# Kernel optimization log

Measured on AMD Instinct MI355X. Metric: run time of the kernel, lower is better.

Reference implementation:

```python
import jax, jax.numpy as jnp
import numpy as np

B, C, N = 2, 512, 2048
HEADS, DIM_HEAD, SCALE = 16, 64, 8.0
H_DIM = HEADS * DIM_HEAD
EPS = 1e-12  # F.normalize default eps


def setup_inputs() -> dict:
    key = jax.random.key(0)
    ks = jax.random.split(key, 5)
    x = jax.random.normal(ks[0], (B, C, N), dtype=jnp.float32)
    Wqkv = jax.random.normal(ks[1], (3 * H_DIM, C), dtype=jnp.float32) * (1.0 / np.sqrt(C))
    q_scale = jnp.ones((DIM_HEAD,), dtype=jnp.float32)
    k_scale = jnp.ones((DIM_HEAD,), dtype=jnp.float32)
    Wout = jax.random.normal(ks[2], (C, H_DIM), dtype=jnp.float32) * (1.0 / np.sqrt(H_DIM))
    bout = jax.random.normal(ks[3], (C,), dtype=jnp.float32) * 0.01
    return {"x": x, "Wqkv": Wqkv, "q_scale": q_scale, "k_scale": k_scale,
            "Wout": Wout, "bout": bout}


def _l2norm(t):
    # F.normalize(t, dim=-1): t / max(||t||, eps)
    n = jnp.sqrt(jnp.sum(t * t, axis=-1, keepdims=True))
    return t / jnp.maximum(n, EPS)


def reference(x, Wqkv, q_scale, k_scale, Wout, bout):
    # 1x1 conv == pointwise matmul over channel dim
    qkv = jnp.einsum('oc,bcn->bon', Wqkv, x)              # [B, 3*H_DIM, N]
    q, k, v = jnp.split(qkv, 3, axis=1)
    # unflatten channels -> [B, H, D, N]
    def to_heads(t):
        return t.reshape(B, HEADS, DIM_HEAD, N)
    q, k, v = map(to_heads, (q, k, v))
    # cosine attention: l2-normalize q,k over head dim, apply learned per-dim scales
    q = _l2norm(q.transpose(0, 1, 3, 2)) * q_scale        # [B, H, N, D]
    k = _l2norm(k.transpose(0, 1, 3, 2)) * k_scale        # [B, H, N, D]
    sim = jnp.einsum('bhid,bhjd->bhij', q, k) * SCALE     # [B, H, N, N]
    attn = jax.nn.softmax(sim, axis=-1)
    out = jnp.einsum('bhij,bhdj->bhid', attn, v)          # [B, H, N, D]
    out = out.transpose(0, 1, 3, 2).reshape(B, H_DIM, N)  # b h n d -> b (h d) n
    return jnp.einsum('oc,bcn->bon', Wout, out) + bout[None, :, None]
```

## Files before the change

### kernel.cpp

```cpp
#include <hip/hip_runtime.h>
#include <hip/hip_bf16.h>

#define BATCH 2
#define CCH   512
#define NSEQ  2048
#define HEADS 16
#define DHEAD 64
#define HDIM  1024
#define ODIM  3072
#define SCALE 8.0f

typedef short short8 __attribute__((ext_vector_type(8)));
typedef float float4v __attribute__((ext_vector_type(4)));

__device__ __forceinline__ float bf2f(unsigned short b) {
    return __uint_as_float(((unsigned int)b) << 16);
}
__device__ __forceinline__ unsigned short f2bf(float f) {
    unsigned int u = __float_as_uint(f);
    return (unsigned short)((u + 0x7FFFu + ((u >> 16) & 1u)) >> 16);
}

typedef __attribute__((address_space(1))) const void* as1_cvp;
typedef __attribute__((address_space(3))) void* as3_vp;
__device__ __forceinline__ void cp16(const void* g, void* l) {
    __builtin_amdgcn_global_load_lds((as1_cvp)g, (as3_vp)l, 16, 0, 0);
}

__global__ __launch_bounds__(64) void k_prep(const float* __restrict__ qs,
                                             const float* __restrict__ ks,
                                             float* __restrict__ M) {
    int lane = threadIdx.x;
    float p = fabsf(qs[lane] * ks[lane]);
#pragma unroll
    for (int off = 1; off < 64; off <<= 1) p = fmaxf(p, __shfl_xor(p, off));
    if (lane == 0) *M = SCALE * p;
}

__global__ __launch_bounds__(256) void k_convert_w(
    const float* __restrict__ Wqkv, const float* __restrict__ Wout,
    unsigned short* __restrict__ Wqkvb, unsigned short* __restrict__ Woutb) {
    int i4 = (blockIdx.x * 256 + threadIdx.x) * 4;
    const float* src; unsigned short* dst; int idx;
    if (i4 < ODIM * CCH) { src = Wqkv; dst = Wqkvb; idx = i4; }
    else { src = Wout; dst = Woutb; idx = i4 - ODIM * CCH; }
    float4 v = *(const float4*)(src + idx);
    ushort4 o;
    o.x = f2bf(v.x); o.y = f2bf(v.y); o.z = f2bf(v.z); o.w = f2bf(v.w);
    *(ushort4*)(dst + idx) = o;
}

__global__ __launch_bounds__(256) void k_transpose_x(
    const float* __restrict__ x, unsigned short* __restrict__ xt) {
    __shared__ unsigned short t[64][65];
    const int b = blockIdx.z, c0 = blockIdx.y * 64, n0 = blockIdx.x * 64;
    const int tr = threadIdx.x >> 6, tc = threadIdx.x & 63;
    const float* xs = x + (size_t)b * CCH * NSEQ;
    unsigned short* xd = xt + (size_t)b * NSEQ * CCH;
#pragma unroll
    for (int r = 0; r < 16; ++r) {
        int c = r * 4 + tr;
        t[c][tc] = f2bf(xs[(size_t)(c0 + c) * NSEQ + n0 + tc]);
    }
    __syncthreads();
#pragma unroll
    for (int r = 0; r < 16; ++r) {
        int n = r * 4 + tr;
        xd[(size_t)(n0 + n) * CCH + c0 + tc] = t[tc][n];
    }
}

__global__ __launch_bounds__(256) void k_gemm_qkv(
    const unsigned short* __restrict__ W, const unsigned short* __restrict__ xt,
    const float* __restrict__ qs, const float* __restrict__ ks,
    unsigned short* __restrict__ qh, unsigned short* __restrict__ kh,
    unsigned short* __restrict__ vb) {
    constexpr int K = CCH, N = NSEQ;
    __shared__ __align__(16) short lsA[128 * 64];
    __shared__ __align__(16) short lsB[128 * 64];
    const int tid = threadIdx.x, wave = tid >> 6, lane = tid & 63;
    const int l15 = lane & 15, quad = lane >> 4;
    const int n0 = blockIdx.x * 128, m0 = blockIdx.y * 128, z = blockIdx.z;
    const short* Ab = (const short*)W + (size_t)m0 * K;
    const short* Bb = (const short*)xt + ((size_t)z * N + n0) * K;
    const int wm = wave >> 1, wn = wave & 1;
    const int cswz = (((tid & 7) ^ ((tid >> 3) & 7))) * 8;
    const int sw7 = (l15 & 7);

    float4v acc[4][4];
#pragma unroll
    for (int i = 0; i < 4; ++i)
#pragma unroll
        for (int j = 0; j < 4; ++j) acc[i][j] = (float4v){0.f, 0.f, 0.f, 0.f};

    for (int k0 = 0; k0 < K; k0 += 64) {
#pragma unroll
        for (int it = 0; it < 4; ++it) {
            int row = it * 32 + (tid >> 3);
            cp16(Ab + (size_t)row * K + k0 + cswz, &lsA[it * 2048 + wave * 512]);
            cp16(Bb + (size_t)row * K + k0 + cswz, &lsB[it * 2048 + wave * 512]);
        }
        __syncthreads();
        short8 af[4][2], bfr[4][2];
#pragma unroll
        for (int t = 0; t < 4; ++t)
#pragma unroll
            for (int kk = 0; kk < 2; ++kk) {
                af[t][kk]  = *(const short8*)&lsA[(wm * 64 + t * 16 + l15) * 64 + ((kk * 4 + quad) ^ sw7) * 8];
                bfr[t][kk] = *(const short8*)&lsB[(wn * 64 + t * 16 + l15) * 64 + ((kk * 4 + quad) ^ sw7) * 8];
            }
#pragma unroll
        for (int mt = 0; mt < 4; ++mt)
#pragma unroll
            for (int nt = 0; nt < 4; ++nt) {
                acc[mt][nt] = __builtin_amdgcn_mfma_f32_16x16x32_bf16(af[mt][0], bfr[nt][0], acc[mt][nt], 0, 0, 0);
                acc[mt][nt] = __builtin_amdgcn_mfma_f32_16x16x32_bf16(af[mt][1], bfr[nt][1], acc[mt][nt], 0, 0, 0);
            }
        __syncthreads();
    }

    const int co   = (m0 + wm * 64) >> 6;
    const int part = co >> 4;
    const int h    = co & 15;
    const int bh   = z * HEADS + h;

    if (part < 2) {
        float inv[4];
#pragma unroll
        for (int nt = 0; nt < 4; ++nt) {
            float ss = 0.f;
#pragma unroll
            for (int mt = 0; mt < 4; ++mt)
#pragma unroll
                for (int r = 0; r < 4; ++r) ss += acc[mt][nt][r] * acc[mt][nt][r];
            ss += __shfl_xor(ss, 16);
            ss += __shfl_xor(ss, 32);
            inv[nt] = 1.0f / fmaxf(sqrtf(ss), 1e-12f);
        }
        const float* sc = part ? ks : qs;
        unsigned short* dst = (part ? kh : qh) + (size_t)bh * NSEQ * DHEAD;
#pragma unroll
        for (int mt = 0; mt < 4; ++mt) {
            const int db = mt * 16 + quad * 4;
            float4 s4 = *(const float4*)(sc + db);
#pragma unroll
            for (int nt = 0; nt < 4; ++nt) {
                int n = n0 + wn * 64 + nt * 16 + l15;
                ushort4 o;
                o.x = f2bf(acc[mt][nt][0] * inv[nt] * s4.x);
                o.y = f2bf(acc[mt][nt][1] * inv[nt] * s4.y);
                o.z = f2bf(acc[mt][nt][2] * inv[nt] * s4.z);
                o.w = f2bf(acc[mt][nt][3] * inv[nt] * s4.w);
                *(ushort4*)(dst + (size_t)n * DHEAD + db) = o;
            }
        }
    } else {
        unsigned short* dst = vb + (size_t)bh * DHEAD * NSEQ;
#pragma unroll
        for (int mt = 0; mt < 4; ++mt)
#pragma unroll
            for (int nt = 0; nt < 4; ++nt) {
                int n = n0 + wn * 64 + nt * 16 + l15;
#pragma unroll
                for (int r = 0; r < 4; ++r) {
                    int d = mt * 16 + quad * 4 + r;
                    dst[(size_t)d * NSEQ + n] = f2bf(acc[mt][nt][r]);
                }
            }
    }
}

__global__ __launch_bounds__(256, 4) void k_attn(
    const unsigned short* __restrict__ qh, const unsigned short* __restrict__ kh,
    const unsigned short* __restrict__ vb,
    float* __restrict__ opart, float* __restrict__ lpart,
    const float* __restrict__ Mptr) {
    __shared__ __align__(16) short Kt[64 * 64];
    __shared__ __align__(16) short Vt[64 * 64];
    __shared__ __align__(16) short Pt[128 * 64];
    const int tid = threadIdx.x, wave = tid >> 6, lane = tid & 63;
    const int l15 = lane & 15, quad = lane >> 4, q8 = quad * 8;
    const int flat = blockIdx.x;
    const int xcd = flat & 7, idx = flat >> 3;
    const int g = (xcd << 3) | (idx >> 4);
    const int i0 = (idx & 15) * 128;
    const int bh = g & 31, z = g >> 5;
    const float Ms = *Mptr;
    const int cswz = (((tid & 7) ^ ((tid >> 3) & 7))) * 8;
    const int sw7 = (l15 & 7);

    short8 qf[2][2];
    const short* qb = (const short*)qh + ((size_t)bh * NSEQ + i0 + wave * 32) * DHEAD;
#pragma unroll
    for (int mt = 0; mt < 2; ++mt)
#pragma unroll
        for (int kt = 0; kt < 2; ++kt)
            qf[mt][kt] = *(const short8*)&qb[(mt * 16 + l15) * DHEAD + kt * 32 + q8];

    float4v of[2][4];
#pragma unroll
    for (int mt = 0; mt < 2; ++mt)
#pragma unroll
        for (int dt = 0; dt < 4; ++dt) of[mt][dt] = (float4v){0.f, 0.f, 0.f, 0.f};
    float l_acc[2][4];
#pragma unroll
    for (int mt = 0; mt < 2; ++mt)
#pragma unroll
        for (int r = 0; r < 4; ++r) l_acc[mt][r] = 0.f;

    const short* kbase = (const short*)kh + (size_t)bh * NSEQ * DHEAD;
    const short* vbase = (const short*)vb + (size_t)bh * DHEAD * NSEQ;

    const int jlo = z * (NSEQ / 2), jhi = jlo + NSEQ / 2;
    for (int j0 = jlo; j0 < jhi; j0 += 64) {
#pragma unroll
        for (int it = 0; it < 2; ++it) {
            int row = it * 32 + (tid >> 3);
            cp16(kbase + (size_t)(j0 + row) * DHEAD + cswz, &Kt[it * 2048 + wave * 512]);
            cp16(vbase + (size_t)row * NSEQ + j0 + cswz, &Vt[it * 2048 + wave * 512]);
        }
        __syncthreads();

        float4v s[2][4];
#pragma unroll
        for (int nt = 0; nt < 4; ++nt) {
            short8 kf0 = *(const short8*)&Kt[(nt * 16 + l15) * 64 + ((0 * 4 + quad) ^ sw7) * 8];
            short8 kf1 = *(const short8*)&Kt[(nt * 16 + l15) * 64 + ((1 * 4 + quad) ^ sw7) * 8];
#pragma unroll
            for (int mt = 0; mt < 2; ++mt) {
                float4v zz = (float4v){0.f, 0.f, 0.f, 0.f};
                zz = __builtin_amdgcn_mfma_f32_16x16x32_bf16(qf[mt][0], kf0, zz, 0, 0, 0);
                zz = __builtin_amdgcn_mfma_f32_16x16x32_bf16(qf[mt][1], kf1, zz, 0, 0, 0);
                s[mt][nt] = zz;
            }
        }

#pragma unroll
        for (int mt = 0; mt < 2; ++mt)
#pragma unroll
            for (int r = 0; r < 4; ++r) {
                int prow = wave * 32 + mt * 16 + quad * 4 + r;
                int psw = (prow & 7);
                float p0 = __expf(fmaf(s[mt][0][r], SCALE, -Ms));
                float p1 = __expf(fmaf(s[mt][1][r], SCALE, -Ms));
                float p2 = __expf(fmaf(s[mt][2][r], SCALE, -Ms));
                float p3 = __expf(fmaf(s[mt][3][r], SCALE, -Ms));
                l_acc[mt][r] += (p0 + p1) + (p2 + p3);
                Pt[prow * 64 + (((0 * 2 + (l15 >> 3)) ^ psw) * 8) + (l15 & 7)] = (short)f2bf(p0);
                Pt[prow * 64 + (((1 * 2 + (l15 >> 3)) ^ psw) * 8) + (l15 & 7)] = (short)f2bf(p1);
                Pt[prow * 64 + (((2 * 2 + (l15 >> 3)) ^ psw) * 8) + (l15 & 7)] = (short)f2bf(p2);
                Pt[prow * 64 + (((3 * 2 + (l15 >> 3)) ^ psw) * 8) + (l15 & 7)] = (short)f2bf(p3);
            }
        __syncthreads();

#pragma unroll
        for (int mt = 0; mt < 2; ++mt) {
            int arow = wave * 32 + mt * 16 + l15;
            short8 af0 = *(const short8*)&Pt[arow * 64 + ((0 * 4 + quad) ^ sw7) * 8];
            short8 af1 = *(const short8*)&Pt[arow * 64 + ((1 * 4 + quad) ^ sw7) * 8];
#pragma unroll
            for (int dt = 0; dt < 4; ++dt) {
                short8 vf0 = *(const short8*)&Vt[(dt * 16 + l15) * 64 + ((0 * 4 + quad) ^ sw7) * 8];
                short8 vf1 = *(const short8*)&Vt[(dt * 16 + l15) * 64 + ((1 * 4 + quad) ^ sw7) * 8];
                of[mt][dt] = __builtin_amdgcn_mfma_f32_16x16x32_bf16(af0, vf0, of[mt][dt], 0, 0, 0);
                of[mt][dt] = __builtin_amdgcn_mfma_f32_16x16x32_bf16(af1, vf1, of[mt][dt], 0, 0, 0);
            }
        }
        __syncthreads();
    }

#pragma unroll
    for (int mt = 0; mt < 2; ++mt)
#pragma unroll
        for (int r = 0; r < 4; ++r) {
            float l = l_acc[mt][r];
#pragma unroll
            for (int off = 1; off < 16; off <<= 1) l += __shfl_xor(l, off);
            l_acc[mt][r] = l;
        }

    float* ob = opart + ((size_t)(z * 32 + bh) * NSEQ) * DHEAD;
    float* lb = lpart + (size_t)(z * 32 + bh) * NSEQ;
#pragma unroll
    for (int mt = 0; mt < 2; ++mt) {
#pragma unroll
        for (int dt = 0; dt < 4; ++dt)
#pragma unroll
            for (int r = 0; r < 4; ++r) {
                int i = i0 + wave * 32 + mt * 16 + quad * 4 + r;
                ob[(size_t)i * DHEAD + dt * 16 + l15] = of[mt][dt][r];
            }
        if (l15 == 0)
#pragma unroll
            for (int r = 0; r < 4; ++r)
                lb[i0 + wave * 32 + mt * 16 + quad * 4 + r] = l_acc[mt][r];
    }
}

__global__ __launch_bounds__(256) void k_merge(
    const float* __restrict__ opart, const float* __restrict__ lpart,
    unsigned short* __restrict__ aot) {
    int t = blockIdx.x * 256 + threadIdx.x;
    int bh = t >> 15, rem = t & 32767;
    int i = rem >> 4, d = (rem & 15) * 4;
    size_t row = (size_t)bh * NSEQ + i;
    const float* o0 = opart;
    const float* o1 = opart + (size_t)32 * NSEQ * DHEAD;
    float l = lpart[row] + lpart[(size_t)32 * NSEQ + row];
    float inv = 1.0f / fmaxf(l, 1e-30f);
    float4 a = *(const float4*)(o0 + row * DHEAD + d);
    float4 b = *(const float4*)(o1 + row * DHEAD + d);
    ushort4 o;
    o.x = f2bf((a.x + b.x) * inv); o.y = f2bf((a.y + b.y) * inv);
    o.z = f2bf((a.z + b.z) * inv); o.w = f2bf((a.w + b.w) * inv);
    int bb = bh >> 4, h = bh & 15;
    *(ushort4*)(aot + ((size_t)bb * NSEQ + i) * HDIM + h * DHEAD + d) = o;
}

__global__ __launch_bounds__(256) void k_gemm_out(
    const unsigned short* __restrict__ W, const unsigned short* __restrict__ aot,
    const float* __restrict__ bias, float* __restrict__ out) {
    constexpr int K = HDIM, N = NSEQ, M = CCH;
    __shared__ __align__(16) short lsA[64 * 64];
    __shared__ __align__(16) short lsB[64 * 64];
    const int tid = threadIdx.x, wave = tid >> 6, lane = tid & 63;
    const int l15 = lane & 15, quad = lane >> 4;
    const int n0 = blockIdx.x * 64, m0 = blockIdx.y * 64, z = blockIdx.z;
    const short* Ab = (const short*)W + (size_t)m0 * K;
    const short* Bb = (const short*)aot + ((size_t)z * N + n0) * K;
    const int wm = wave >> 1, wn = wave & 1;
    const int cswz = (((tid & 7) ^ ((tid >> 3) & 7))) * 8;
    const int sw7 = (l15 & 7);

    float4v acc[2][2];
#pragma unroll
    for (int i = 0; i < 2; ++i)
#pragma unroll
        for (int j = 0; j < 2; ++j) acc[i][j] = (float4v){0.f, 0.f, 0.f, 0.f};

    for (int k0 = 0; k0 < K; k0 += 64) {
        {
            int row = tid >> 3;
            cp16(Ab + (size_t)row * K + k0 + cswz, &lsA[wave * 512]);
            cp16(Ab + (size_t)(row + 32) * K + k0 + cswz, &lsA[2048 + wave * 512]);
            cp16(Bb + (size_t)row * K + k0 + cswz, &lsB[wave * 512]);
            cp16(Bb + (size_t)(row + 32) * K + k0 + cswz, &lsB[2048 + wave * 512]);
        }
        __syncthreads();
        short8 af[2][2], bfr[2][2];
#pragma unroll
        for (int t = 0; t < 2; ++t)
#pragma unroll
            for (int kk = 0; kk < 2; ++kk) {
                af[t][kk]  = *(const short8*)&lsA[(wm * 32 + t * 16 + l15) * 64 + ((kk * 4 + quad) ^ sw7) * 8];
                bfr[t][kk] = *(const short8*)&lsB[(wn * 32 + t * 16 + l15) * 64 + ((kk * 4 + quad) ^ sw7) * 8];
            }
#pragma unroll
        for (int mt = 0; mt < 2; ++mt)
#pragma unroll
            for (int nt = 0; nt < 2; ++nt) {
                acc[mt][nt] = __builtin_amdgcn_mfma_f32_16x16x32_bf16(af[mt][0], bfr[nt][0], acc[mt][nt], 0, 0, 0);
                acc[mt][nt] = __builtin_amdgcn_mfma_f32_16x16x32_bf16(af[mt][1], bfr[nt][1], acc[mt][nt], 0, 0, 0);
            }
        __syncthreads();
    }
    float* Co = out + (size_t)z * M * N;
#pragma unroll
    for (int mt = 0; mt < 2; ++mt)
#pragma unroll
        for (int nt = 0; nt < 2; ++nt) {
            int mrow = m0 + wm * 32 + mt * 16 + quad * 4;
#pragma unroll
            for (int r = 0; r < 4; ++r) {
                int mr = mrow + r;
                int nc = n0 + wn * 32 + nt * 16 + l15;
                Co[(size_t)mr * N + nc] = acc[mt][nt][r] + bias[mr];
            }
        }
}

extern "C" void kernel_launch(void* const* d_in, const int* in_sizes, int n_in,
                              void* d_out, int out_size, void* d_ws, size_t ws_size,
                              hipStream_t stream) {
    const float* x = nullptr; const float* Wqkv = nullptr;
    const float* qs = nullptr; const float* ks = nullptr;
    const float* Wout = nullptr; const float* bout = nullptr;
    for (int i = 0; i < n_in; ++i) {
        switch (in_sizes[i]) {
            case BATCH * CCH * NSEQ: x    = (const float*)d_in[i]; break;
            case ODIM * CCH:         Wqkv = (const float*)d_in[i]; break;
            case CCH * HDIM:         Wout = (const float*)d_in[i]; break;
            case CCH:                bout = (const float*)d_in[i]; break;
            case DHEAD: if (!qs) qs = (const float*)d_in[i]; else ks = (const float*)d_in[i]; break;
            default: break;
        }
    }
    float* y = (float*)d_out;

    char* ws = (char*)d_ws;
    float*          Mbuf  = (float*)(ws + 0);
    unsigned short* Wqkvb = (unsigned short*)(ws + 4096);
    unsigned short* Woutb = (unsigned short*)(ws + 3149824);
    unsigned short* xt    = (unsigned short*)(ws + 4198400);
    unsigned short* qh    = (unsigned short*)(ws + 8392704);
    unsigned short* kh    = (unsigned short*)(ws + 16781312);
    unsigned short* vb    = (unsigned short*)(ws + 25169920);
    unsigned short* aot   = (unsigned short*)(ws + 33558528);
    float*          opart = (float*)(ws + 41947136);
    float*          lpart = (float*)(ws + 75501568);

    k_prep<<<1, 64, 0, stream>>>(qs, ks, Mbuf);
    k_convert_w<<<(ODIM * CCH + CCH * HDIM) / 4 / 256, 256, 0, stream>>>(Wqkv, Wout, Wqkvb, Woutb);
    k_transpose_x<<<dim3(NSEQ / 64, CCH / 64, BATCH), 256, 0, stream>>>(x, xt);
    k_gemm_qkv<<<dim3(NSEQ / 128, ODIM / 128, BATCH), 256, 0, stream>>>(Wqkvb, xt, qs, ks, qh, kh, vb);
    k_attn<<<dim3(1024), 256, 0, stream>>>(qh, kh, vb, opart, lpart, Mbuf);
    k_merge<<<dim3(BATCH * HEADS * NSEQ * (DHEAD / 4) / 256), 256, 0, stream>>>(opart, lpart, aot);
    k_gemm_out<<<dim3(NSEQ / 64, CCH / 64, BATCH), 256, 0, stream>>>(Woutb, aot, bout, y);
}
```

Baseline: 174.3 us.

## Fold softmax scale into Q, use exp2 with max-init MFMA, stage QKV stores

Q is pre-multiplied by SCALE*log2(e) in the QKV epilogue, and the MFMA accumulator starts at -M. Together these turn each softmax exponent into a bare exp2 with no fma, and bf16 rounding of P uses a cheaper round-half-up conversion. The QKV GEMM epilogue now stages its outputs through LDS, so Q/K rows and transposed V are written as coalesced 16-byte stores instead of scattered 2-byte writes. The separate k_prep launch is merged into k_convert_w. Rounding Q after the prescale and the simpler bf16 rounding slightly change numerics.

Measured after the change: 176.8 us. Within noise of the previous version (+1.4%).

```diff
diff --git a/kernel.cpp b/kernel.cpp
--- a/kernel.cpp
+++ b/kernel.cpp
@@ -8,17 +8,25 @@
 #define DHEAD 64
 #define HDIM  1024
 #define ODIM  3072
-#define SCALE 8.0f
-
+#define QK_PRESCALE 11.541560327111707f
+
+typedef short short4v __attribute__((ext_vector_type(4)));
 typedef short short8 __attribute__((ext_vector_type(8)));
 typedef float float4v __attribute__((ext_vector_type(4)));
 
-__device__ __forceinline__ float bf2f(unsigned short b) {
-    return __uint_as_float(((unsigned int)b) << 16);
-}
 __device__ __forceinline__ unsigned short f2bf(float f) {
     unsigned int u = __float_as_uint(f);
     return (unsigned short)((u + 0x7FFFu + ((u >> 16) & 1u)) >> 16);
+}
+__device__ __forceinline__ unsigned short f2bf_fast(float f) {
+    return (unsigned short)((__float_as_uint(f) + 0x8000u) >> 16);
+}
+__device__ __forceinline__ float fexp2(float x) {
+#if __has_builtin(__builtin_amdgcn_exp2f)
+    return __builtin_amdgcn_exp2f(x);
+#else
+    return exp2f(x);
+#endif
 }
 
 typedef __attribute__((address_space(1))) const void* as1_cvp;
@@ -27,19 +35,18 @@
     __builtin_amdgcn_global_load_lds((as1_cvp)g, (as3_vp)l, 16, 0, 0);
 }
 
-__global__ __launch_bounds__(64) void k_prep(const float* __restrict__ qs,
-                                             const float* __restrict__ ks,
-                                             float* __restrict__ M) {
-    int lane = threadIdx.x;
-    float p = fabsf(qs[lane] * ks[lane]);
-#pragma unroll
-    for (int off = 1; off < 64; off <<= 1) p = fmaxf(p, __shfl_xor(p, off));
-    if (lane == 0) *M = SCALE * p;
-}
-
 __global__ __launch_bounds__(256) void k_convert_w(
     const float* __restrict__ Wqkv, const float* __restrict__ Wout,
-    unsigned short* __restrict__ Wqkvb, unsigned short* __restrict__ Woutb) {
+    const float* __restrict__ qs, const float* __restrict__ ks,
+    unsigned short* __restrict__ Wqkvb, unsigned short* __restrict__ Woutb,
+    float* __restrict__ M) {
+    if (blockIdx.x == 0 && threadIdx.x < 64) {
+        int lane = threadIdx.x;
+        float p = fabsf(qs[lane] * ks[lane]);
+#pragma unroll
+        for (int off = 1; off < 64; off <<= 1) p = fmaxf(p, __shfl_xor(p, off));
+        if (lane == 0) *M = QK_PRESCALE * p;
+    }
     int i4 = (blockIdx.x * 256 + threadIdx.x) * 4;
     const float* src; unsigned short* dst; int idx;
     if (i4 < ODIM * CCH) { src = Wqkv; dst = Wqkvb; idx = i4; }
@@ -76,8 +83,9 @@
     unsigned short* __restrict__ qh, unsigned short* __restrict__ kh,
     unsigned short* __restrict__ vb) {
     constexpr int K = CCH, N = NSEQ;
-    __shared__ __align__(16) short lsA[128 * 64];
-    __shared__ __align__(16) short lsB[128 * 64];
+    __shared__ __align__(16) short smem[2 * 128 * 64];
+    short* lsA = smem;
+    short* lsB = smem + 128 * 64;
     const int tid = threadIdx.x, wave = tid >> 6, lane = tid & 63;
     const int l15 = lane & 15, quad = lane >> 4;
     const int n0 = blockIdx.x * 128, m0 = blockIdx.y * 128, z = blockIdx.z;
@@ -123,6 +131,7 @@
     const int part = co >> 4;
     const int h    = co & 15;
     const int bh   = z * HEADS + h;
+    short* myT = smem + wave * 4096;
 
     if (part < 2) {
         float inv[4];
@@ -138,35 +147,51 @@
             inv[nt] = 1.0f / fmaxf(sqrtf(ss), 1e-12f);
         }
         const float* sc = part ? ks : qs;
-        unsigned short* dst = (part ? kh : qh) + (size_t)bh * NSEQ * DHEAD;
+        const float csc = part ? 1.0f : QK_PRESCALE;
 #pragma unroll
         for (int mt = 0; mt < 4; ++mt) {
             const int db = mt * 16 + quad * 4;
             float4 s4 = *(const float4*)(sc + db);
+            s4.x *= csc; s4.y *= csc; s4.z *= csc; s4.w *= csc;
 #pragma unroll
             for (int nt = 0; nt < 4; ++nt) {
-                int n = n0 + wn * 64 + nt * 16 + l15;
-                ushort4 o;
-                o.x = f2bf(acc[mt][nt][0] * inv[nt] * s4.x);
-                o.y = f2bf(acc[mt][nt][1] * inv[nt] * s4.y);
-                o.z = f2bf(acc[mt][nt][2] * inv[nt] * s4.z);
-                o.w = f2bf(acc[mt][nt][3] * inv[nt] * s4.w);
-                *(ushort4*)(dst + (size_t)n * DHEAD + db) = o;
-            }
+                int nl = nt * 16 + l15;
+                short4v o;
+                o.x = (short)f2bf(acc[mt][nt][0] * inv[nt] * s4.x);
+                o.y = (short)f2bf(acc[mt][nt][1] * inv[nt] * s4.y);
+                o.z = (short)f2bf(acc[mt][nt][2] * inv[nt] * s4.z);
+                o.w = (short)f2bf(acc[mt][nt][3] * inv[nt] * s4.w);
+                *(short4v*)&myT[nl * 64 + (((db >> 3) ^ (nl & 7)) << 3) + (db & 7)] = o;
+            }
+        }
+        unsigned short* dst = (part ? kh : qh) + (size_t)bh * NSEQ * DHEAD
+                              + (size_t)(n0 + wn * 64) * DHEAD;
+#pragma unroll
+        for (int pass = 0; pass < 8; ++pass) {
+            int nl = pass * 8 + (lane >> 3), c = lane & 7;
+            short8 vv = *(const short8*)&myT[nl * 64 + ((c ^ (nl & 7)) << 3)];
+            *(short8*)&dst[(size_t)nl * DHEAD + c * 8] = vv;
         }
     } else {
-        unsigned short* dst = vb + (size_t)bh * DHEAD * NSEQ;
 #pragma unroll
         for (int mt = 0; mt < 4; ++mt)
 #pragma unroll
             for (int nt = 0; nt < 4; ++nt) {
-                int n = n0 + wn * 64 + nt * 16 + l15;
+                int nl = nt * 16 + l15;
+                int swc = nl >> 3, swo = nl & 7;
 #pragma unroll
                 for (int r = 0; r < 4; ++r) {
                     int d = mt * 16 + quad * 4 + r;
-                    dst[(size_t)d * NSEQ + n] = f2bf(acc[mt][nt][r]);
+                    myT[d * 64 + ((swc ^ (d & 7)) << 3) + swo] = (short)f2bf(acc[mt][nt][r]);
                 }
             }
+        unsigned short* dst = vb + (size_t)bh * DHEAD * NSEQ + n0 + wn * 64;
+#pragma unroll
+        for (int pass = 0; pass < 8; ++pass) {
+            int d = pass * 8 + (lane >> 3), c = lane & 7;
+            short8 vv = *(const short8*)&myT[d * 64 + ((c ^ (d & 7)) << 3)];
+            *(short8*)&dst[(size_t)d * NSEQ + c * 8] = vv;
+        }
     }
 }
 
@@ -186,6 +211,7 @@
     const int i0 = (idx & 15) * 128;
     const int bh = g & 31, z = g >> 5;
     const float Ms = *Mptr;
+    const float4v mInit = (float4v){-Ms, -Ms, -Ms, -Ms};
     const int cswz = (((tid & 7) ^ ((tid >> 3) & 7))) * 8;
     const int sw7 = (l15 & 7);
 
@@ -228,7 +254,7 @@
             short8 kf1 = *(const short8*)&Kt[(nt * 16 + l15) * 64 + ((1 * 4 + quad) ^ sw7) * 8];
 #pragma unroll
             for (int mt = 0; mt < 2; ++mt) {
-                float4v zz = (float4v){0.f, 0.f, 0.f, 0.f};
+                float4v zz = mInit;
                 zz = __builtin_amdgcn_mfma_f32_16x16x32_bf16(qf[mt][0], kf0, zz, 0, 0, 0);
                 zz = __builtin_amdgcn_mfma_f32_16x16x32_bf16(qf[mt][1], kf1, zz, 0, 0, 0);
                 s[mt][nt] = zz;
@@ -241,15 +267,15 @@
             for (int r = 0; r < 4; ++r) {
                 int prow = wave * 32 + mt * 16 + quad * 4 + r;
                 int psw = (prow & 7);
-                float p0 = __expf(fmaf(s[mt][0][r], SCALE, -Ms));
-                float p1 = __expf(fmaf(s[mt][1][r], SCALE, -Ms));
-                float p2 = __expf(fmaf(s[mt][2][r], SCALE, -Ms));
-                float p3 = __expf(fmaf(s[mt][3][r], SCALE, -Ms));
+                float p0 = fexp2(s[mt][0][r]);
+                float p1 = fexp2(s[mt][1][r]);
+                float p2 = fexp2(s[mt][2][r]);
+                float p3 = fexp2(s[mt][3][r]);
                 l_acc[mt][r] += (p0 + p1) + (p2 + p3);
-                Pt[prow * 64 + (((0 * 2 + (l15 >> 3)) ^ psw) * 8) + (l15 & 7)] = (short)f2bf(p0);
-                Pt[prow * 64 + (((1 * 2 + (l15 >> 3)) ^ psw) * 8) + (l15 & 7)] = (short)f2bf(p1);
-                Pt[prow * 64 + (((2 * 2 + (l15 >> 3)) ^ psw) * 8) + (l15 & 7)] = (short)f2bf(p2);
-                Pt[prow * 64 + (((3 * 2 + (l15 >> 3)) ^ psw) * 8) + (l15 & 7)] = (short)f2bf(p3);
+                Pt[prow * 64 + (((0 * 2 + (l15 >> 3)) ^ psw) * 8) + (l15 & 7)] = (short)f2bf_fast(p0);
+                Pt[prow * 64 + (((1 * 2 + (l15 >> 3)) ^ psw) * 8) + (l15 & 7)] = (short)f2bf_fast(p1);
+                Pt[prow * 64 + (((2 * 2 + (l15 >> 3)) ^ psw) * 8) + (l15 & 7)] = (short)f2bf_fast(p2);
+                Pt[prow * 64 + (((3 * 2 + (l15 >> 3)) ^ psw) * 8) + (l15 & 7)] = (short)f2bf_fast(p3);
             }
         __syncthreads();
 
@@ -409,8 +435,8 @@
     float*          opart = (float*)(ws + 41947136);
     float*          lpart = (float*)(ws + 75501568);
 
-    k_prep<<<1, 64, 0, stream>>>(qs, ks, Mbuf);
-    k_convert_w<<<(ODIM * CCH + CCH * HDIM) / 4 / 256, 256, 0, stream>>>(Wqkv, Wout, Wqkvb, Woutb);
+    k_convert_w<<<(ODIM * CCH + CCH * HDIM) / 4 / 256, 256, 0, stream>>>(
+        Wqkv, Wout, qs, ks, Wqkvb, Woutb, Mbuf);
     k_transpose_x<<<dim3(NSEQ / 64, CCH / 64, BATCH), 256, 0, stream>>>(x, xt);
     k_gemm_qkv<<<dim3(NSEQ / 128, ODIM / 128, BATCH), 256, 0, stream>>>(Wqkvb, xt, qs, ks, qh, kh, vb);
     k_attn<<<dim3(1024), 256, 0, stream>>>(qh, kh, vb, opart, lpart, Mbuf);
```
